# Performance work log

Hardware: AMD Instinct MI355X
Metric: run time of the kernel (lower is better)

Reference implementation:

```python
import jax, jax.numpy as jnp
import numpy as np

K_HOPS = 2
IMPROVED = False  # self-loop fill weight = 1.0


def setup_inputs() -> dict:
    key = jax.random.key(0)
    k1, k2, k3 = jax.random.split(key, 3)
    n_nodes, n_edges, d_feat, units = 100000, 1600000, 64, 64
    x = jax.random.normal(k1, (n_nodes, d_feat), dtype=jnp.float32)
    edge_index = jax.random.randint(k2, (2, n_edges), 0, n_nodes, dtype=jnp.int32)
    edge_weight = jnp.ones((n_edges,), dtype=jnp.float32)
    kernel = jax.random.normal(k3, (d_feat, units), dtype=jnp.float32) * (1.0 / np.sqrt(d_feat))
    bias = jnp.zeros((units,), dtype=jnp.float32)
    return {"x": x, "edge_index": edge_index, "edge_weight": edge_weight,
            "kernel": kernel, "bias": bias}


def reference(x, edge_index, edge_weight, kernel, bias):
    n = x.shape[0]
    # renorm trick: add self-loops (fill=1, or 2 if improved) BEFORE normalization
    fill = jnp.float32(2.0 if IMPROVED else 1.0)
    loop_idx = jnp.arange(n, dtype=edge_index.dtype)
    row = jnp.concatenate([edge_index[0], loop_idx])
    col = jnp.concatenate([edge_index[1], loop_idx])
    w = jnp.concatenate([edge_weight, jnp.full((n,), fill, dtype=edge_weight.dtype)])
    # symmetric GCN normalization: D^{-1/2} A D^{-1/2}
    deg = jax.ops.segment_sum(w, row, num_segments=n)
    dinv = jnp.where(deg > 0, jax.lax.rsqrt(deg), 0.0)
    norm_w = dinv[row] * w * dinv[col]  # [n_edges + n]
    # K-hop propagation: gather source feats, scale, scatter-add to targets
    h = x
    for _ in range(K_HOPS):
        msgs = h[col] * norm_w[:, None]           # [E+n, d] gather + scale
        h = jax.ops.segment_sum(msgs, row, num_segments=n)  # scatter-add
    # final dense projection
    return h @ kernel + bias
```

## Files before the change

### kernel.cpp

```cpp
#include <hip/hip_runtime.h>

#define D 64

static __host__ __device__ inline int alignup(int x) { return (x + 63) & ~63; }

__device__ inline float blo(unsigned int u) { return __uint_as_float(u << 16); }
__device__ inline float bhi(unsigned int u) { return __uint_as_float(u & 0xffff0000u); }
__device__ inline unsigned short f2b(float f) {
    unsigned int u = __float_as_uint(f);
    return (unsigned short)((u + 0x7FFFu + ((u >> 16) & 1u)) >> 16);
}
__device__ inline unsigned int packb(float lo, float hi) {
    return (unsigned int)f2b(lo) | ((unsigned int)f2b(hi) << 16);
}

typedef short bf16x8 __attribute__((ext_vector_type(8)));
typedef float f32x4 __attribute__((ext_vector_type(4)));

__global__ void convert_bf16(const float* __restrict__ x, unsigned short* __restrict__ xb, long nElem) {
    long t = (long)blockIdx.x * blockDim.x + threadIdx.x;
    long i = t * 4;
    if (i + 3 < nElem) {
        float4 v = *(const float4*)(x + i);
        ushort4 o;
        o.x = f2b(v.x); o.y = f2b(v.y); o.z = f2b(v.z); o.w = f2b(v.w);
        *(ushort4*)(xb + i) = o;
    } else {
        for (long k = i; k < nElem; ++k) xb[k] = f2b(x[k]);
    }
}

__global__ void convert_wbt(const float* __restrict__ W, unsigned short* __restrict__ wbt) {
    int idx = blockIdx.x * blockDim.x + threadIdx.x;
    int c = idx >> 6, k = idx & 63;
    wbt[c * 64 + k] = f2b(W[k * 64 + c]);
}

__global__ void countA(const int* __restrict__ row, int* __restrict__ bhist,
                       int E, int chunk, int NB) {
    __shared__ int h[512];
    int b = blockIdx.x;
    for (int k = threadIdx.x; k < NB; k += blockDim.x) h[k] = 0;
    __syncthreads();
    int s = b * chunk, e = min(s + chunk, E);
    for (int p = s + (int)threadIdx.x; p < e; p += blockDim.x)
        atomicAdd(&h[row[p] >> 8], 1);
    __syncthreads();
    for (int k = threadIdx.x; k < NB; k += blockDim.x)
        bhist[k * 256 + b] = h[k];
}

__global__ void scanA(int* __restrict__ bhist, int* __restrict__ bcnt, int NB) {
    __shared__ int s[256];
    int k = blockIdx.x;
    int t = threadIdx.x;
    int v = bhist[k * 256 + t];
    s[t] = v;
    __syncthreads();
    for (int o = 1; o < 256; o <<= 1) {
        int u = (t >= o) ? s[t - o] : 0;
        __syncthreads();
        if (t >= o) s[t] += u;
        __syncthreads();
    }
    bhist[k * 256 + t] = s[t] - v;
    if (t == 255) bcnt[k] = s[t];
}

__global__ void scan_boff(const int* __restrict__ bcnt, int* __restrict__ boff, int nb) {
    __shared__ int s[512];
    int t = threadIdx.x;
    s[t] = (t < nb) ? bcnt[t] : 0;
    __syncthreads();
    for (int o = 1; o < 512; o <<= 1) {
        int v = (t >= o) ? s[t - o] : 0;
        __syncthreads();
        if (t >= o) s[t] += v;
        __syncthreads();
    }
    if (t < nb) boff[t] = (t == 0) ? 0 : s[t - 1];
}

__global__ void scatterB(const int* __restrict__ row, const int* __restrict__ col,
                         const float* __restrict__ w, const int* __restrict__ bhist,
                         const int* __restrict__ boff, uint2* __restrict__ ebuf,
                         int E, int chunk, int NB) {
    __shared__ int cur[512];
    int b = blockIdx.x;
    for (int k = threadIdx.x; k < NB; k += blockDim.x)
        cur[k] = boff[k] + bhist[k * 256 + b];
    __syncthreads();
    int s = b * chunk, e = min(s + chunk, E);
    for (int p = s + (int)threadIdx.x; p < e; p += blockDim.x) {
        int r = row[p];
        int bkt = r >> 8;
        int pos = atomicAdd(&cur[bkt], 1);
        ebuf[pos] = make_uint2(((unsigned)(r & 255) << 24) | (unsigned)col[p],
                               __float_as_uint(w[p]));
    }
}

__global__ void fineC1(const uint2* __restrict__ ebuf, const int* __restrict__ boff,
                       const int* __restrict__ bcnt, int* __restrict__ cnt, int n) {
    __shared__ int c2[256];
    int k = blockIdx.x;
    c2[threadIdx.x] = 0;
    __syncthreads();
    int s = boff[k], e = s + bcnt[k];
    for (int p = s + (int)threadIdx.x; p < e; p += blockDim.x)
        atomicAdd(&c2[ebuf[p].x >> 24], 1);
    __syncthreads();
    int r = k * 256 + threadIdx.x;
    if (r < n) cnt[r] = c2[threadIdx.x];
}

__global__ void placeC2(const uint2* __restrict__ ebuf, const int* __restrict__ boff,
                        const int* __restrict__ bcnt, const int* __restrict__ off,
                        uint2* __restrict__ csr, int n) {
    __shared__ int c2[256];
    int k = blockIdx.x;
    c2[threadIdx.x] = 0;
    __syncthreads();
    int s = boff[k], e = s + bcnt[k];
    for (int p = s + (int)threadIdx.x; p < e; p += blockDim.x) {
        uint2 ent = ebuf[p];
        int rl = (int)(ent.x >> 24);
        int pos = atomicAdd(&c2[rl], 1);
        int r = k * 256 + rl;
        csr[off[r] + pos] = make_uint2(ent.x & 0xFFFFFFu, ent.y);
    }
}

__global__ void scan_block_sums(const int* __restrict__ cnt, int* __restrict__ bsums, int n) {
    __shared__ int s[256];
    int t = threadIdx.x;
    int i = blockIdx.x * 256 + t;
    s[t] = (i < n) ? cnt[i] : 0;
    __syncthreads();
    for (int st = 128; st > 0; st >>= 1) {
        if (t < st) s[t] += s[t + st];
        __syncthreads();
    }
    if (t == 0) bsums[blockIdx.x] = s[0];
}

__global__ void scan_bsums(int* __restrict__ bsums, int nb) {
    __shared__ int s[1024];
    int t = threadIdx.x;
    s[t] = (t < nb) ? bsums[t] : 0;
    __syncthreads();
    for (int off = 1; off < 1024; off <<= 1) {
        int v = 0;
        if (t >= off) v = s[t - off];
        __syncthreads();
        if (t >= off) s[t] += v;
        __syncthreads();
    }
    if (t < nb) bsums[t] = (t == 0) ? 0 : s[t - 1];
}

__global__ void scan_final(const int* __restrict__ cnt, const int* __restrict__ bsums,
                           int* __restrict__ off, int* __restrict__ end, int n) {
    __shared__ int s[256];
    int t = threadIdx.x;
    int i = blockIdx.x * 256 + t;
    int v = (i < n) ? cnt[i] : 0;
    s[t] = v;
    __syncthreads();
    for (int o = 1; o < 256; o <<= 1) {
        int u = 0;
        if (t >= o) u = s[t - o];
        __syncthreads();
        if (t >= o) s[t] += u;
        __syncthreads();
    }
    if (i < n) {
        int o0 = bsums[blockIdx.x] + s[t] - v;
        off[i] = o0;
        end[i] = o0 + v;
    }
}

__global__ void seg_dinv(const uint2* __restrict__ csr, const int* __restrict__ off,
                         const int* __restrict__ end, float* __restrict__ dinv,
                         int n, float fill) {
    int i = blockIdx.x * blockDim.x + threadIdx.x;
    if (i >= n) return;
    float d = fill;
    int s = off[i], e = end[i];
    for (int p = s; p < e; ++p) d += __uint_as_float(csr[p].y);
    dinv[i] = d > 0.0f ? rsqrtf(d) : 0.0f;
}

__global__ void norm_w(uint2* __restrict__ csr, const int* __restrict__ off,
                       const int* __restrict__ end, const float* __restrict__ dinv, int n) {
    int i = blockIdx.x * blockDim.x + threadIdx.x;
    if (i >= n) return;
    float di = dinv[i];
    int s = off[i], e = end[i];
    for (int p = s; p < e; ++p) {
        uint2 ent = csr[p];
        float wn = __uint_as_float(ent.y) * di * dinv[(int)ent.x];
        ((float*)csr)[2 * p + 1] = wn;
    }
}

__global__ void __launch_bounds__(256)
__attribute__((amdgpu_waves_per_eu(2, 4)))
hop_g8(const unsigned short* __restrict__ xb, const float* __restrict__ dinv,
       const int* __restrict__ off, const int* __restrict__ end,
       const uint2* __restrict__ csr,
       unsigned short* __restrict__ outb, int n) {
    int t = blockIdx.x * blockDim.x + threadIdx.x;
    int wave = t >> 6;
    int lane = t & 63;
    int g = lane >> 3, q = lane & 7;
    int i = wave * 8 + g;
    bool active = i < n;
    int ii = active ? i : n - 1;

    const unsigned int* xw = (const unsigned int*)xb;
    float di = dinv[ii];
    float di2 = di * di;
    uint4 sv = *(const uint4*)(xw + (long)ii * 32 + q * 4);
    float a0 = blo(sv.x) * di2, a1 = bhi(sv.x) * di2;
    float a2 = blo(sv.y) * di2, a3 = bhi(sv.y) * di2;
    float a4 = blo(sv.z) * di2, a5 = bhi(sv.z) * di2;
    float a6 = blo(sv.w) * di2, a7 = bhi(sv.w) * di2;

    int s = active ? off[ii] : 0;
    int e = active ? end[ii] : 0;

    for (int b = s; b < e; b += 16) {
        int i0 = b + q;     if (i0 >= e) i0 = e - 1;
        int i1 = b + 8 + q; if (i1 >= e) i1 = e - 1;
        uint2 e0 = csr[i0];
        uint2 e1 = csr[i1];
        uint4 v[16];
        float wv[16];
        #pragma unroll
        for (int j = 0; j < 16; ++j) {
            int srcl = g * 8 + (j & 7);
            int cb = __shfl((int)(j < 8 ? e0.x : e1.x), srcl, 64);
            float wj = __uint_as_float(__shfl((int)(j < 8 ? e0.y : e1.y), srcl, 64));
            if (b + j >= e) wj = 0.0f;
            wv[j] = wj;
            v[j] = make_uint4(0u, 0u, 0u, 0u);
            if (wj != 0.0f) v[j] = *(const uint4*)(xw + (long)cb * 32 + q * 4);
        }
        #pragma unroll
        for (int j = 0; j < 16; ++j) {
            float wj = wv[j];
            a0 += blo(v[j].x) * wj; a1 += bhi(v[j].x) * wj;
            a2 += blo(v[j].y) * wj; a3 += bhi(v[j].y) * wj;
            a4 += blo(v[j].z) * wj; a5 += bhi(v[j].z) * wj;
            a6 += blo(v[j].w) * wj; a7 += bhi(v[j].w) * wj;
        }
    }

    if (!active) return;
    uint4 o;
    o.x = packb(a0, a1); o.y = packb(a2, a3);
    o.z = packb(a4, a5); o.w = packb(a6, a7);
    *(uint4*)((unsigned int*)outb + (long)i * 32 + q * 4) = o;
}

__global__ void __launch_bounds__(256)
proj_mfma(const unsigned short* __restrict__ h2b, const unsigned short* __restrict__ wbt,
          const float* __restrict__ bias, float* __restrict__ out, int n) {
    int lane = threadIdx.x & 63;
    int w = (blockIdx.x * blockDim.x + threadIdx.x) >> 6;
    int nTiles = (n + 15) >> 4;
    if (w >= nTiles) return;
    int r0 = w * 16;
    int rl = lane & 15;
    int half = lane >> 4;

    int ar = r0 + rl; if (ar >= n) ar = n - 1;
    const unsigned short* arow = h2b + (long)ar * 64 + half * 8;
    bf16x8 A0 = __builtin_bit_cast(bf16x8, *(const uint4*)(arow));
    bf16x8 A1 = __builtin_bit_cast(bf16x8, *(const uint4*)(arow + 32));

    #pragma unroll
    for (int t = 0; t < 4; ++t) {
        const unsigned short* bcol = wbt + (long)(t * 16 + rl) * 64 + half * 8;
        bf16x8 B0 = __builtin_bit_cast(bf16x8, *(const uint4*)(bcol));
        bf16x8 B1 = __builtin_bit_cast(bf16x8, *(const uint4*)(bcol + 32));
        float bl = bias[t * 16 + rl];
        f32x4 acc = {bl, bl, bl, bl};
        acc = __builtin_amdgcn_mfma_f32_16x16x32_bf16(A0, B0, acc, 0, 0, 0);
        acc = __builtin_amdgcn_mfma_f32_16x16x32_bf16(A1, B1, acc, 0, 0, 0);
        #pragma unroll
        for (int j = 0; j < 4; ++j) {
            int r = r0 + half * 4 + j;
            if (r < n) out[(long)r * 64 + t * 16 + rl] = acc[j];
        }
    }
}

extern "C" void kernel_launch(void* const* d_in, const int* in_sizes, int n_in,
                              void* d_out, int out_size, void* d_ws, size_t ws_size,
                              hipStream_t stream) {
    const float* x    = (const float*)d_in[0];
    const int*   ei   = (const int*)d_in[1];
    const float* ew   = (const float*)d_in[2];
    const float* W    = (const float*)d_in[3];
    const float* bias = (const float*)d_in[4];

    int n = in_sizes[0] / D;
    int E = in_sizes[2];
    const int* row = ei;
    const int* col = ei + E;

    float* out = (float*)d_out;

    const int NB = (n + 255) >> 8;
    const int BA = 256;
    int chunk = (E + BA - 1) / BA;

    float* dinv  = (float*)d_ws;
    int*   cnt   = (int*)(dinv + alignup(n));
    int*   bsums = cnt + alignup(n);
    int*   off   = bsums + 1024;
    int*   endp  = off + alignup(n);
    int*   bcnt  = endp + alignup(n);
    int*   boff  = bcnt + 512;
    int*   bhist = boff + 512;
    uint2* csr   = (uint2*)(bhist + alignup(NB * 256));
    unsigned short* xb  = (unsigned short*)(csr + alignup(E));
    unsigned short* h1b = xb + (long)alignup(n) * D;
    unsigned short* h2b = h1b + (long)alignup(n) * D;
    unsigned short* wbt = h2b + (long)alignup(n) * D;
    uint2* ebuf = (uint2*)h2b;

    const float fill = 1.0f;
    const int blk = 256;
    int nbN = (n + blk - 1) / blk;

    long nElem = (long)n * D;
    int nbC = (int)((nElem / 4 + blk - 1) / blk);
    convert_bf16<<<nbC, blk, 0, stream>>>(x, xb, nElem);
    convert_wbt<<<16, 256, 0, stream>>>(W, wbt);

    countA<<<BA, 256, 0, stream>>>(row, bhist, E, chunk, NB);
    scanA<<<NB, 256, 0, stream>>>(bhist, bcnt, NB);
    scan_boff<<<1, 512, 0, stream>>>(bcnt, boff, NB);
    scatterB<<<BA, 256, 0, stream>>>(row, col, ew, bhist, boff, ebuf, E, chunk, NB);
    fineC1<<<NB, 256, 0, stream>>>(ebuf, boff, bcnt, cnt, n);
    scan_block_sums<<<nbN, blk, 0, stream>>>(cnt, bsums, n);
    scan_bsums<<<1, 1024, 0, stream>>>(bsums, nbN);
    scan_final<<<nbN, blk, 0, stream>>>(cnt, bsums, off, endp, n);
    placeC2<<<NB, 256, 0, stream>>>(ebuf, boff, bcnt, off, csr, n);

    seg_dinv<<<nbN, blk, 0, stream>>>(csr, off, endp, dinv, n, fill);
    norm_w<<<nbN, blk, 0, stream>>>(csr, off, endp, dinv, n);

    int nWaves = (n + 7) / 8;
    int nbHop = (nWaves * 64 + blk - 1) / blk;
    hop_g8<<<nbHop, blk, 0, stream>>>(xb, dinv, off, endp, csr, h1b, n);
    hop_g8<<<nbHop, blk, 0, stream>>>(h1b, dinv, off, endp, csr, h2b, n);

    int nTiles = (n + 15) / 16;
    int nbProj = (nTiles * 64 + blk - 1) / blk;
    proj_mfma<<<nbProj, blk, 0, stream>>>(h2b, wbt, bias, out, n);
}
```

Baseline: 188.2 us.

## Fuse CSR fine-bucket count, scan, placement and degree into one kernel

Merges the per-bucket count, three-kernel global scan, placement, and degree/dinv computation into a single bucketC kernel. It uses the coarse bucket offsets plus a local shared-memory scan, so no global per-node scan is needed. Normalization now runs per bucket and reads the row dinv from shared memory, with edge-parallel coalesced access instead of per-node serial loops. The two conversion kernels are also merged into one launch. The cost is fewer launches and fewer passes over the edge list, in exchange for shared-memory float atomics whose summation order is nondeterministic.

```diff
diff --git a/kernel.cpp b/kernel.cpp
--- a/kernel.cpp
+++ b/kernel.cpp
@@ -17,7 +17,15 @@
 typedef short bf16x8 __attribute__((ext_vector_type(8)));
 typedef float f32x4 __attribute__((ext_vector_type(4)));
 
-__global__ void convert_bf16(const float* __restrict__ x, unsigned short* __restrict__ xb, long nElem) {
+__global__ void convert_all(const float* __restrict__ x, unsigned short* __restrict__ xb,
+                            const float* __restrict__ W, unsigned short* __restrict__ wbt,
+                            long nElem, int nbC) {
+    if ((int)blockIdx.x >= nbC) {
+        int idx = ((int)blockIdx.x - nbC) * 256 + threadIdx.x;
+        int c = idx >> 6, k = idx & 63;
+        wbt[c * 64 + k] = f2b(W[k * 64 + c]);
+        return;
+    }
     long t = (long)blockIdx.x * blockDim.x + threadIdx.x;
     long i = t * 4;
     if (i + 3 < nElem) {
@@ -30,11 +38,6 @@
     }
 }
 
-__global__ void convert_wbt(const float* __restrict__ W, unsigned short* __restrict__ wbt) {
-    int idx = blockIdx.x * blockDim.x + threadIdx.x;
-    int c = idx >> 6, k = idx & 63;
-    wbt[c * 64 + k] = f2b(W[k * 64 + c]);
-}
 
 __global__ void countA(const int* __restrict__ row, int* __restrict__ bhist,
                        int E, int chunk, int NB) {
@@ -100,108 +103,68 @@
     }
 }
 
-__global__ void fineC1(const uint2* __restrict__ ebuf, const int* __restrict__ boff,
-                       const int* __restrict__ bcnt, int* __restrict__ cnt, int n) {
-    __shared__ int c2[256];
+__global__ void bucketC(const uint2* __restrict__ ebuf, const int* __restrict__ boff,
+                        const int* __restrict__ bcnt, float* __restrict__ dinv,
+                        int* __restrict__ off, int* __restrict__ endp,
+                        uint2* __restrict__ csr, int n, float fill) {
+    __shared__ int cntS[256];
+    __shared__ float wsum[256];
+    __shared__ int scanS[256];
+    __shared__ int cur[256];
     int k = blockIdx.x;
-    c2[threadIdx.x] = 0;
+    int t = threadIdx.x;
+    cntS[t] = 0;
+    wsum[t] = 0.f;
     __syncthreads();
     int s = boff[k], e = s + bcnt[k];
-    for (int p = s + (int)threadIdx.x; p < e; p += blockDim.x)
-        atomicAdd(&c2[ebuf[p].x >> 24], 1);
-    __syncthreads();
-    int r = k * 256 + threadIdx.x;
-    if (r < n) cnt[r] = c2[threadIdx.x];
-}
-
-__global__ void placeC2(const uint2* __restrict__ ebuf, const int* __restrict__ boff,
-                        const int* __restrict__ bcnt, const int* __restrict__ off,
-                        uint2* __restrict__ csr, int n) {
-    __shared__ int c2[256];
-    int k = blockIdx.x;
-    c2[threadIdx.x] = 0;
-    __syncthreads();
-    int s = boff[k], e = s + bcnt[k];
-    for (int p = s + (int)threadIdx.x; p < e; p += blockDim.x) {
+    for (int p = s + t; p < e; p += 256) {
         uint2 ent = ebuf[p];
         int rl = (int)(ent.x >> 24);
-        int pos = atomicAdd(&c2[rl], 1);
-        int r = k * 256 + rl;
-        csr[off[r] + pos] = make_uint2(ent.x & 0xFFFFFFu, ent.y);
-    }
-}
-
-__global__ void scan_block_sums(const int* __restrict__ cnt, int* __restrict__ bsums, int n) {
-    __shared__ int s[256];
+        atomicAdd(&cntS[rl], 1);
+        atomicAdd(&wsum[rl], __uint_as_float(ent.y));
+    }
+    __syncthreads();
+    int r = k * 256 + t;
+    int v = cntS[t];
+    if (r < n) {
+        float d = fill + wsum[t];
+        dinv[r] = d > 0.0f ? rsqrtf(d) : 0.0f;
+    }
+    scanS[t] = v;
+    __syncthreads();
+    for (int o = 1; o < 256; o <<= 1) {
+        int u = (t >= o) ? scanS[t - o] : 0;
+        __syncthreads();
+        if (t >= o) scanS[t] += u;
+        __syncthreads();
+    }
+    int base = boff[k] + scanS[t] - v;
+    cur[t] = base;
+    if (r < n) { off[r] = base; endp[r] = base + v; }
+    __syncthreads();
+    for (int p = s + t; p < e; p += 256) {
+        uint2 ent = ebuf[p];
+        int rl = (int)(ent.x >> 24);
+        int pos = atomicAdd(&cur[rl], 1);
+        csr[pos] = ent;
+    }
+}
+
+__global__ void normB(uint2* __restrict__ csr, const int* __restrict__ boff,
+                      const int* __restrict__ bcnt, const float* __restrict__ dinv, int n) {
+    __shared__ float dl[256];
+    int k = blockIdx.x;
     int t = threadIdx.x;
-    int i = blockIdx.x * 256 + t;
-    s[t] = (i < n) ? cnt[i] : 0;
-    __syncthreads();
-    for (int st = 128; st > 0; st >>= 1) {
-        if (t < st) s[t] += s[t + st];
-        __syncthreads();
-    }
-    if (t == 0) bsums[blockIdx.x] = s[0];
-}
-
-__global__ void scan_bsums(int* __restrict__ bsums, int nb) {
-    __shared__ int s[1024];
-    int t = threadIdx.x;
-    s[t] = (t < nb) ? bsums[t] : 0;
-    __syncthreads();
-    for (int off = 1; off < 1024; off <<= 1) {
-        int v = 0;
-        if (t >= off) v = s[t - off];
-        __syncthreads();
-        if (t >= off) s[t] += v;
-        __syncthreads();
-    }
-    if (t < nb) bsums[t] = (t == 0) ? 0 : s[t - 1];
-}
-
-__global__ void scan_final(const int* __restrict__ cnt, const int* __restrict__ bsums,
-                           int* __restrict__ off, int* __restrict__ end, int n) {
-    __shared__ int s[256];
-    int t = threadIdx.x;
-    int i = blockIdx.x * 256 + t;
-    int v = (i < n) ? cnt[i] : 0;
-    s[t] = v;
-    __syncthreads();
-    for (int o = 1; o < 256; o <<= 1) {
-        int u = 0;
-        if (t >= o) u = s[t - o];
-        __syncthreads();
-        if (t >= o) s[t] += u;
-        __syncthreads();
-    }
-    if (i < n) {
-        int o0 = bsums[blockIdx.x] + s[t] - v;
-        off[i] = o0;
-        end[i] = o0 + v;
-    }
-}
-
-__global__ void seg_dinv(const uint2* __restrict__ csr, const int* __restrict__ off,
-                         const int* __restrict__ end, float* __restrict__ dinv,
-                         int n, float fill) {
-    int i = blockIdx.x * blockDim.x + threadIdx.x;
-    if (i >= n) return;
-    float d = fill;
-    int s = off[i], e = end[i];
-    for (int p = s; p < e; ++p) d += __uint_as_float(csr[p].y);
-    dinv[i] = d > 0.0f ? rsqrtf(d) : 0.0f;
-}
-
-__global__ void norm_w(uint2* __restrict__ csr, const int* __restrict__ off,
-                       const int* __restrict__ end, const float* __restrict__ dinv, int n) {
-    int i = blockIdx.x * blockDim.x + threadIdx.x;
-    if (i >= n) return;
-    float di = dinv[i];
-    int s = off[i], e = end[i];
-    for (int p = s; p < e; ++p) {
+    int r = k * 256 + t;
+    dl[t] = (r < n) ? dinv[r] : 0.f;
+    __syncthreads();
+    int s = boff[k], e = s + bcnt[k];
+    for (int p = s + t; p < e; p += 256) {
         uint2 ent = csr[p];
-        float wn = __uint_as_float(ent.y) * di * dinv[(int)ent.x];
-        ((float*)csr)[2 * p + 1] = wn;
+        int rl = (int)(ent.x >> 24);
+        unsigned c = ent.x & 0xFFFFFFu;
+        float wn = __uint_as_float(ent.y) * dl[rl] * dinv[c];
+        csr[p] = make_uint2(c, __float_as_uint(wn));
     }
 }
 
@@ -319,9 +282,7 @@
     int chunk = (E + BA - 1) / BA;
 
     float* dinv  = (float*)d_ws;
-    int*   cnt   = (int*)(dinv + alignup(n));
-    int*   bsums = cnt + alignup(n);
-    int*   off   = bsums + 1024;
+    int*   off   = (int*)(dinv + alignup(n));
     int*   endp  = off + alignup(n);
     int*   bcnt  = endp + alignup(n);
     int*   boff  = bcnt + 512;
@@ -335,25 +296,17 @@
 
     const float fill = 1.0f;
     const int blk = 256;
-    int nbN = (n + blk - 1) / blk;
 
     long nElem = (long)n * D;
     int nbC = (int)((nElem / 4 + blk - 1) / blk);
-    convert_bf16<<<nbC, blk, 0, stream>>>(x, xb, nElem);
-    convert_wbt<<<16, 256, 0, stream>>>(W, wbt);
+    convert_all<<<nbC + 16, blk, 0, stream>>>(x, xb, W, wbt, nElem, nbC);
 
     countA<<<BA, 256, 0, stream>>>(row, bhist, E, chunk, NB);
     scanA<<<NB, 256, 0, stream>>>(bhist, bcnt, NB);
     scan_boff<<<1, 512, 0, stream>>>(bcnt, boff, NB);
     scatterB<<<BA, 256, 0, stream>>>(row, col, ew, bhist, boff, ebuf, E, chunk, NB);
-    fineC1<<<NB, 256, 0, stream>>>(ebuf, boff, bcnt, cnt, n);
-    scan_block_sums<<<nbN, blk, 0, stream>>>(cnt, bsums, n);
-    scan_bsums<<<1, 1024, 0, stream>>>(bsums, nbN);
-    scan_final<<<nbN, blk, 0, stream>>>(cnt, bsums, off, endp, n);
-    placeC2<<<NB, 256, 0, stream>>>(ebuf, boff, bcnt, off, csr, n);
-
-    seg_dinv<<<nbN, blk, 0, stream>>>(csr, off, endp, dinv, n, fill);
-    norm_w<<<nbN, blk, 0, stream>>>(csr, off, endp, dinv, n);
+    bucketC<<<NB, 256, 0, stream>>>(ebuf, boff, bcnt, dinv, off, endp, csr, n, fill);
+    normB<<<NB, 256, 0, stream>>>(csr, boff, bcnt, dinv, n);
 
     int nWaves = (n + 7) / 8;
     int nbHop = (nWaves * 64 + blk - 1) / blk;
```

Result: faster. 159.7 us (-15.1%).
